# Performance work log

Measured on AMD Instinct MI355X. Metric: run time of the kernel, lower is better.

The kernel has to match this reference:

```python
import jax, jax.numpy as jnp
import numpy as np

N_NODES = 30522
HID = 768
N_EDGES = 488352
B, S = 4, 512
L = 12  # transformer_layers
C = 100  # num classes in pos-neg codebook graph


def setup_inputs() -> dict:
    key = jax.random.key(0)
    ks = jax.random.split(key, 20)
    inp = {}
    inp["word_embs"] = jax.random.normal(ks[0], (N_NODES, HID), dtype=jnp.float32)
    inp["input_ids"] = jax.random.randint(ks[1], (B, S), 0, N_NODES + 1)  # N_NODES = padding row
    inp["class_ids"] = jax.random.randint(ks[2], (B, S), 0, C + 1)
    inp["mask"] = jax.random.randint(ks[3], (B, S, 1), 0, 2).astype(bool)
    inp["co_edge_index"] = jax.random.randint(ks[4], (2, N_EDGES), 0, N_NODES)
    inp["co_edge_weight"] = jax.random.uniform(ks[5], (N_EDGES,), dtype=jnp.float32)
    inp["re_edge_index"] = jax.random.randint(ks[6], (2, N_EDGES), 0, N_NODES)
    inp["re_edge_weight"] = jax.random.uniform(ks[7], (N_EDGES,), dtype=jnp.float32)
    pn_graph = jax.random.uniform(ks[8], (C + 1, N_NODES), dtype=jnp.float32) * 0.01
    inp["pn_graph"] = pn_graph.at[-1].set(0.0)  # padding row of zeros
    sc = 0.02
    inp["co_W"] = jax.random.normal(ks[9], (3, HID, HID), dtype=jnp.float32) * sc
    inp["co_b"] = jnp.zeros((3, HID), jnp.float32)
    inp["re_W"] = jax.random.normal(ks[10], (3, HID, HID), dtype=jnp.float32) * sc
    inp["re_b"] = jnp.zeros((3, HID), jnp.float32)
    inp["pn_W"] = jax.random.normal(ks[11], (HID, HID), dtype=jnp.float32) * sc  # [out,in] 1x1 conv
    inp["pn_b"] = jnp.zeros((HID,), jnp.float32)
    # zero_convs are zero-initialized in the original; use small random so math is non-trivial
    inp["zero_w"] = jax.random.normal(ks[12], (L, HID, HID), dtype=jnp.float32) * sc
    inp["zero_b"] = jnp.zeros((L, HID), jnp.float32)
    inp["zero_w_pos"] = jax.random.normal(ks[13], (L, HID, HID), dtype=jnp.float32) * sc
    inp["zero_b_pos"] = jnp.zeros((L, HID), jnp.float32)
    return inp


def _gcn_layer(x, src, dst, ew, W, b, n):
    # PyG GCNConv: add self-loops (weight 1), symmetric normalization
    deg = jax.ops.segment_sum(ew, dst, num_segments=n) + 1.0
    dinv = jnp.where(deg > 0, jax.lax.rsqrt(deg), 0.0)
    norm = dinv[src] * ew * dinv[dst]  # [E]
    h = x @ W  # [n, H]
    agg = jax.ops.segment_sum(norm[:, None] * h[src], dst, num_segments=n)
    agg = agg + h * (dinv * dinv)[:, None]  # self-loop contribution
    return agg + b


def _gcn_stack(x, edge_index, ew, Ws, bs, ids):
    src, dst = edge_index[0], edge_index[1]
    n = x.shape[0]
    h = x
    acc = None
    for i in range(3):
        h = jax.nn.relu(_gcn_layer(h, src, dst, ew, Ws[i], bs[i], n))
        pad = jnp.concatenate([h, jnp.zeros((1, h.shape[-1]), h.dtype)], axis=0)
        g = pad[ids]  # [B, S, H] gather with padding row
        acc = g if acc is None else acc + g
    return acc / 3.0


def _zero_conv_layers(tok, w, b):
    # 1x1 conv over hidden channels for each of L layers: [B,S,H] x [L,O,H] -> [L,B,S,O]
    return jnp.einsum("bsh,loh->lbso", tok, w) + b[:, None, None, :]


def reference(word_embs, input_ids, class_ids, mask,
              co_edge_index, co_edge_weight, re_edge_index, re_edge_weight,
              pn_graph, co_W, co_b, re_W, re_b, pn_W, pn_b,
              zero_w, zero_b, zero_w_pos, zero_b_pos):
    Bq, Sq = input_ids.shape
    H = word_embs.shape[-1]
    Lq = zero_w.shape[0]
    inv_mask = (~mask).astype(word_embs.dtype)  # [B,S,1]
    zero_pad = jnp.zeros((Lq, Bq, 1, H), word_embs.dtype)

    co = _gcn_stack(word_embs, co_edge_index, co_edge_weight, co_W, co_b, input_ids)  # [B,S,H]
    re = _gcn_stack(word_embs, re_edge_index, re_edge_weight, re_W, re_b, input_ids)

    # NOTE: original uses self.zero_convs (not a separate set) for BOTH co and re
    co_l = _zero_conv_layers(co, zero_w, zero_b) * inv_mask[None]
    re_l = _zero_conv_layers(re, zero_w, zero_b) * inv_mask[None]
    co_l = jnp.concatenate([zero_pad, co_l], axis=2)  # [L,B,S+1,H]
    re_l = jnp.concatenate([zero_pad, re_l], axis=2)

    # PosNegCodebook: 1x1 conv on codebook, then dense-graph matmul, gathered by class
    cb = word_embs @ pn_W.T + pn_b  # [N, H]
    pn = (pn_graph @ cb)[class_ids]  # [B,S,H] (same math as graph[class_ids] @ cb)
    pn_l = _zero_conv_layers(pn, zero_w_pos, zero_b_pos)
    pn_l = jnp.concatenate([zero_pad, pn_l], axis=2)

    return (co_l, re_l, pn_l)
```

## Files before the change

kernel.cpp:

```cpp
#include <hip/hip_runtime.h>
#include <stdint.h>

typedef unsigned int u32;
typedef unsigned short u16;
typedef __attribute__((ext_vector_type(8))) short short8;
typedef __attribute__((ext_vector_type(4))) float f32x4;

#define N_NODESC 30522
#define HIDC 768
#define NEC 488352
#define TOKM 2048
#define LLAY 12
#define NCLS 101
#define M_PAD 30720
#define ZNC (LLAY*HIDC)
#define OUT_SET (LLAY*4*513*HIDC)
#define PN_KCHUNK 512
#define NBLK 120
#define NN1 (N_NODESC+1)
#define G4_LDS 65536
#define G8_LDS 131072

__device__ __forceinline__ float bl(u32 u){ return __uint_as_float(u<<16); }
__device__ __forceinline__ float bh(u32 u){ return __uint_as_float(u & 0xffff0000u); }
__device__ __forceinline__ u32 f2b1(float f){ u32 x=__float_as_uint(f); return (x + 0x7fffu + ((x>>16)&1u))>>16; }
__device__ __forceinline__ u32 pack2(float a, float b){ return f2b1(a) | (f2b1(b)<<16); }

__device__ __forceinline__ void mfma16(f32x4& d, short8 a, short8 b){
  asm volatile("v_mfma_f32_16x16x32_bf16 %0, %1, %2, %0" : "+v"(d) : "v"(a), "v"(b));
}
__device__ __forceinline__ void async16(const void* g, void* l){
  __builtin_amdgcn_global_load_lds((const __attribute__((address_space(1))) u32*)g,
                                   (__attribute__((address_space(3))) u32*)l, 16, 0, 0);
}
__device__ __forceinline__ void em_dec(double d, int& s, float& w){
  unsigned long long b = __double_as_longlong(d);
  s = (int)(u32)b;
  w = __uint_as_float((u32)(b>>32));
}

__global__ void k_invmask(const void* __restrict__ mask, float* __restrict__ invm){
  __shared__ int s_byte, s_flt;
  int t = threadIdx.x;
  const unsigned char* mb = (const unsigned char*)mask;
  const u32* mw = (const u32*)mask;
  int lb=0, lf=0;
  for(int i=t;i<2048;i+=256) if((i&3)!=0 && mb[i]!=0) lb=1;
  for(int i=t;i<512;i+=256) if(mw[i]==0x3F800000u) lf=1;
  if(t==0){ s_byte=0; s_flt=0; }
  __syncthreads();
  if(lb) s_byte=1;
  if(lf) s_flt=1;
  __syncthreads();
  int mode = s_flt ? 2 : (s_byte ? 1 : 0);
  for(int p=t;p<2048;p+=256){
    int mv = (mode==1) ? (int)mb[p] : (int)(mw[p]!=0u);
    invm[p] = mv ? 0.f : 1.f;
  }
}

__global__ void k_needed(const int* __restrict__ ids, u32* __restrict__ needed,
                         u32* __restrict__ need1,
                         int* __restrict__ tmap, int* __restrict__ nxt){
  int p = blockIdx.x*256 + threadIdx.x;
  if(p < TOKM){
    int id = ids[p];
    if(id < N_NODESC){
      needed[id] = 1u;
      need1[id] = 1u;
      need1[N_NODESC + id] = 1u;
      int old = atomicExch(&tmap[id], p);
      nxt[p] = old;
    }
  }
}

__global__ void k_need_expand(const int* __restrict__ coei, const int* __restrict__ reei,
                              const u32* __restrict__ needed, u32* __restrict__ need1){
  int g = blockIdx.y;
  const int* ei = g ? reei : coei;
  int e = blockIdx.x*256 + threadIdx.x;
  if(e < NEC){
    int d = ei[NEC+e];
    if(needed[d]) need1[(size_t)g*N_NODESC + ei[e]] = 1u;
  }
}

__global__ void k_convAll(const float* __restrict__ pnW, const float* __restrict__ zw,
                          const float* __restrict__ zwp,
                          u16* __restrict__ pnwb, u16* __restrict__ zwall){
  const int NP = HIDC*HIDC/2;
  const int NZ = ZNC*HIDC/2;
  int i = blockIdx.x*256 + threadIdx.x;
  if(i < NP){
    ((u32*)pnwb)[i] = pack2(pnW[2*i], pnW[2*i+1]);
  } else if(i < NP + NZ){
    int j = i - NP;
    ((u32*)zwall)[j] = pack2(zw[2*j], zw[2*j+1]);
  } else if(i < NP + 2*NZ){
    int j = i - NP - NZ;
    ((u32*)zwall)[NZ + j] = pack2(zwp[2*j], zwp[2*j+1]);
  }
}
__global__ void k_conv_pad(const float* __restrict__ src, u16* __restrict__ dst, int srcRows, int padRows){
  int i = blockIdx.x*256 + threadIdx.x;
  if(i >= padRows*384) return;
  int row = i/384; int c2 = (i - row*384)*2;
  float lo=0.f, hi=0.f;
  if(row < srcRows){ const float* s = src + (size_t)row*HIDC + c2; lo=s[0]; hi=s[1]; }
  ((u32*)dst)[i] = pack2(lo, hi);
}
__global__ void k_pnb(const float* __restrict__ png, u16* __restrict__ pnb){
  int i = blockIdx.x*256 + threadIdx.x;
  if(i >= 128*(M_PAD/2)) return;
  int row = i/(M_PAD/2); int k2 = (i - row*(M_PAD/2))*2;
  float lo=0.f, hi=0.f;
  if(row < NCLS){
    const float* s = png + (size_t)row*N_NODESC;
    if(k2 < N_NODESC) lo = s[k2];
    if(k2+1 < N_NODESC) hi = s[k2+1];
  }
  ((u32*)pnb)[i] = pack2(lo, hi);
}
__global__ void k_transposeW2(const float* __restrict__ coW, const float* __restrict__ reW,
                              u16* __restrict__ Wt2){
  int g = blockIdx.y;
  int i = blockIdx.x*256 + threadIdx.x;
  if(i >= 3*HIDC*384) return;
  const float* W = g ? reW : coW;
  int mat = i/(HIDC*384); int rem = i - mat*HIDC*384;
  int n = rem/384; int kd = rem - n*384;
  const float* Wm = W + (size_t)mat*HIDC*HIDC;
  float lo = Wm[(size_t)(2*kd)*HIDC + n];
  float hi = Wm[(size_t)(2*kd+1)*HIDC + n];
  ((u32*)Wt2)[(size_t)g*3*HIDC*384 + (size_t)mat*HIDC*384 + (size_t)n*384 + kd] = pack2(lo, hi);
}

__global__ void k_degcnt2(const int* __restrict__ coei, const int* __restrict__ reei,
                          const float* __restrict__ coew, const float* __restrict__ reew,
                          float* __restrict__ deg2, int* __restrict__ cnt2){
  int g = blockIdx.y;
  const int* ei = g ? reei : coei;
  const float* ew = g ? reew : coew;
  int e = blockIdx.x*256 + threadIdx.x;
  if(e < NEC){ int d = ei[NEC+e]; atomicAdd(&deg2[(size_t)g*N_NODESC + d], ew[e]); atomicAdd(&cnt2[(size_t)g*N_NODESC + d], 1); }
}
__global__ void k_scan1(const int* __restrict__ cnt2, int* __restrict__ part2,
                        const float* __restrict__ deg2,
                        float* __restrict__ dinvA, float* __restrict__ dinvB){
  __shared__ int wt[4];
  int g = blockIdx.y, b = blockIdx.x, t = threadIdx.x;
  int lane = t & 63, w = t >> 6;
  int i = b*256 + t;
  if(i < N_NODESC){
    float d = deg2[(size_t)g*N_NODESC + i] + 1.f;
    dinvA[(size_t)g*N_NODESC + i] = rsqrtf(d);
    dinvB[(size_t)g*N_NODESC + i] = 1.f/d;
  }
  int v = (i < N_NODESC) ? cnt2[(size_t)g*N_NODESC + i] : 0;
  int x = v;
  #pragma unroll
  for(int off=1; off<64; off<<=1){ int y = __shfl_up(x, off); if(lane>=off) x += y; }
  if(lane==63) wt[w] = x;
  __syncthreads();
  if(t==0) part2[g*NBLK + b] = wt[0]+wt[1]+wt[2]+wt[3];
}
__global__ void k_scan2(int* __restrict__ part2, int* __restrict__ rp2){
  __shared__ int w0tot;
  int g = blockIdx.x, t = threadIdx.x;
  int lane = t & 63, w = t >> 6;
  int v = (t < NBLK) ? part2[g*NBLK + t] : 0;
  int x = v;
  #pragma unroll
  for(int off=1; off<64; off<<=1){ int y = __shfl_up(x, off); if(lane>=off) x += y; }
  if(w==0 && lane==63) w0tot = x;
  __syncthreads();
  int incl = x + (w ? w0tot : 0);
  int excl = incl - v;
  if(t < NBLK) part2[g*NBLK + t] = excl;
  if(t == 127) rp2[(size_t)g*NN1 + N_NODESC] = incl;
}
__global__ void k_scan3(const int* __restrict__ cnt2, const int* __restrict__ part2,
                        int* __restrict__ rp2, int* __restrict__ cur2){
  __shared__ int wt[4];
  int g = blockIdx.y, b = blockIdx.x, t = threadIdx.x;
  int lane = t & 63, w = t >> 6;
  int i = b*256 + t;
  int v = (i < N_NODESC) ? cnt2[(size_t)g*N_NODESC + i] : 0;
  int x = v;
  #pragma unroll
  for(int off=1; off<64; off<<=1){ int y = __shfl_up(x, off); if(lane>=off) x += y; }
  if(lane==63) wt[w] = x;
  __syncthreads();
  int wpre = 0;
  #pragma unroll
  for(int j=0;j<4;j++) if(j<w) wpre += wt[j];
  int excl = x - v + wpre + part2[g*NBLK + b];
  if(i < N_NODESC){ rp2[(size_t)g*NN1 + i] = excl; cur2[(size_t)g*N_NODESC + i] = excl; }
}
__global__ void k_scatter2(const int* __restrict__ coei, const int* __restrict__ reei,
                           const float* __restrict__ coew, const float* __restrict__ reew,
                           const float* __restrict__ dinvA, int* __restrict__ cur2,
                           float2* __restrict__ emeta){
  int g = blockIdx.y;
  const int* ei = g ? reei : coei;
  const float* ew = g ? reew : coew;
  int e = blockIdx.x*256 + threadIdx.x;
  if(e < NEC){
    int s = ei[e], d = ei[NEC+e];
    int pos = atomicAdd(&cur2[(size_t)g*N_NODESC + d], 1);
    float nrm = dinvA[(size_t)g*N_NODESC + s]*ew[e]*dinvA[(size_t)g*N_NODESC + d];
    emeta[(size_t)g*NEC + pos] = make_float2(__int_as_float(s), nrm);
  }
}

__global__ __launch_bounds__(256)
void k_spmm(const u16* __restrict__ hW, const int* __restrict__ rp,
            const float2* __restrict__ emeta, const float* __restrict__ dinv2,
            const float* __restrict__ bias, u16* __restrict__ hout,
            const u32* __restrict__ needed,
            const int* __restrict__ tmap, const int* __restrict__ nxt,
            float2* __restrict__ tokf, u16* __restrict__ tokb, int phase){
  int v = blockIdx.x*4 + (threadIdx.x>>6);
  if(v >= N_NODESC) return;
  if(needed && !needed[v]) return;
  int lane = threadIdx.x & 63;
  const u32* H = (const u32*)hW;
  const double* em8 = (const double*)emeta;
  float acc[12];
  #pragma unroll
  for(int q=0;q<12;q++) acc[q]=0.f;
  int e0 = rp[v], e1 = rp[v+1];
  int e = e0;
  for(; e+8<=e1; e+=8){
    int s[8]; float w[8];
    #pragma unroll
    for(int j=0;j<8;j++) em_dec(__builtin_nontemporal_load(em8+e+j), s[j], w[j]);
    const u32* r[8];
    #pragma unroll
    for(int j=0;j<8;j++) r[j] = H + (size_t)s[j]*384 + lane;
    u32 u[8][6];
    #pragma unroll
    for(int j=0;j<8;j++){
      #pragma unroll
      for(int q=0;q<6;q++) u[j][q] = r[j][q*64];
    }
    #pragma unroll
    for(int q=0;q<6;q++){
      acc[2*q]   += w[0]*bl(u[0][q]) + w[1]*bl(u[1][q]) + w[2]*bl(u[2][q]) + w[3]*bl(u[3][q]);
      acc[2*q+1] += w[0]*bh(u[0][q]) + w[1]*bh(u[1][q]) + w[2]*bh(u[2][q]) + w[3]*bh(u[3][q]);
      acc[2*q]   += w[4]*bl(u[4][q]) + w[5]*bl(u[5][q]) + w[6]*bl(u[6][q]) + w[7]*bl(u[7][q]);
      acc[2*q+1] += w[4]*bh(u[4][q]) + w[5]*bh(u[5][q]) + w[6]*bh(u[6][q]) + w[7]*bh(u[7][q]);
    }
  }
  for(; e+4<=e1; e+=4){
    int s0,s1,s2,s3; float w0,w1,w2,w3;
    em_dec(__builtin_nontemporal_load(em8+e  ), s0, w0);
    em_dec(__builtin_nontemporal_load(em8+e+1), s1, w1);
    em_dec(__builtin_nontemporal_load(em8+e+2), s2, w2);
    em_dec(__builtin_nontemporal_load(em8+e+3), s3, w3);
    const u32* r0 = H + (size_t)s0*384 + lane;
    const u32* r1 = H + (size_t)s1*384 + lane;
    const u32* r2 = H + (size_t)s2*384 + lane;
    const u32* r3 = H + (size_t)s3*384 + lane;
    u32 u0[6],u1[6],u2[6],u3[6];
    #pragma unroll
    for(int q=0;q<6;q++){ u0[q]=r0[q*64]; u1[q]=r1[q*64]; u2[q]=r2[q*64]; u3[q]=r3[q*64]; }
    #pragma unroll
    for(int q=0;q<6;q++){
      acc[2*q]   += w0*bl(u0[q]) + w1*bl(u1[q]) + w2*bl(u2[q]) + w3*bl(u3[q]);
      acc[2*q+1] += w0*bh(u0[q]) + w1*bh(u1[q]) + w2*bh(u2[q]) + w3*bh(u3[q]);
    }
  }
  for(; e<e1; ++e){
    int ss; float ww;
    em_dec(__builtin_nontemporal_load(em8+e), ss, ww);
    const u32* r = H + (size_t)ss*384 + lane;
    #pragma unroll
    for(int q=0;q<6;q++){ u32 u = r[q*64]; acc[2*q] += ww*bl(u); acc[2*q+1] += ww*bh(u); }
  }
  { float wgt = dinv2[v];
    const u32* r = H + (size_t)v*384 + lane;
    #pragma unroll
    for(int q=0;q<6;q++){ u32 u = r[q*64]; acc[2*q] += wgt*bl(u); acc[2*q+1] += wgt*bh(u); }
  }
  const float2* B2 = (const float2*)bias;
  u32 wv[6];
  #pragma unroll
  for(int q=0;q<6;q++){
    float2 bb = B2[lane + 64*q];
    float x0 = fmaxf(acc[2*q]+bb.x, 0.f);
    float x1 = fmaxf(acc[2*q+1]+bb.y, 0.f);
    wv[q] = pack2(x0, x1);
  }
  if(phase != 2){
    u32* O = (u32*)hout + (size_t)v*384 + lane;
    #pragma unroll
    for(int q=0;q<6;q++) O[q*64] = wv[q];
  }
  int p = tmap[v];
  while(p >= 0){
    float2* TF = tokf + (size_t)p*384 + lane;
    if(phase == 0){
      #pragma unroll
      for(int q=0;q<6;q++)
        TF[q*64] = make_float2(bl(wv[q])*(1.f/3.f), bh(wv[q])*(1.f/3.f));
    } else if(phase == 1){
      #pragma unroll
      for(int q=0;q<6;q++){
        float2 c = TF[q*64];
        c.x += bl(wv[q])*(1.f/3.f); c.y += bh(wv[q])*(1.f/3.f);
        TF[q*64] = c;
      }
    } else {
      u32* TB = (u32*)tokb + (size_t)p*384 + lane;
      #pragma unroll
      for(int q=0;q<6;q++){
        float2 c = TF[q*64];
        c.x += bl(wv[q])*(1.f/3.f); c.y += bh(wv[q])*(1.f/3.f);
        TB[q*64] = pack2(c.x, c.y);
      }
    }
    p = nxt[p];
  }
}

__global__ void k_gather_pn(const float* __restrict__ GT, const int* __restrict__ cids, u16* __restrict__ tokb){
  int d = blockIdx.x*256 + threadIdx.x;
  if(d >= TOKM*384) return;
  int p = d/384, q = d - p*384;
  int cid = cids[p];
  float lo = GT[(size_t)(2*q)*128 + cid];
  float hi = GT[(size_t)(2*q+1)*128 + cid];
  ((u32*)tokb)[d] = pack2(lo, hi);
}

__global__ void k_zerocol(float* __restrict__ out){
  int i = blockIdx.x*256 + threadIdx.x;
  if(i >= 3*LLAY*4*HIDC) return;
  int set = i/(LLAY*4*HIDC); int rem = i - set*(LLAY*4*HIDC);
  int l = rem/(4*HIDC); int rem2 = rem - l*(4*HIDC);
  int b = rem2/HIDC; int o = rem2 - b*HIDC;
  out[(size_t)set*OUT_SET + (size_t)(l*4+b)*513*HIDC + o] = 0.f;
}

__device__ __forceinline__ void g_split(int ntM, int ntN, int& bm, int& bn){
  int nwg = ntM*ntN;
  int bid = (int)blockIdx.x;
  int wg = (bid & 7)*(nwg>>3) + (bid>>3);
  if(ntN <= ntM){ bm = wg/ntN; bn = wg - bm*ntN; }
  else          { bn = wg/ntM; bm = wg - bn*ntM; }
}

#define G8_AOFF(b) ((b)*65536)
#define G8_BOFF(b) ((b)*65536 + 32768)

__device__ __forceinline__ void g8_stage(const u16* __restrict__ src, int ldk, int g0, int kt,
                                         char* half_base, int tid){
  const int lane = tid & 63;
  const int csw = ((lane&7) ^ (lane>>3)) << 3;
  const u16* s0 = src + (size_t)(g0 + (tid>>3))*ldk + (kt + csw);
  const u16* s1 = src + (size_t)(g0 + 64 + (tid>>3))*ldk + (kt + csw);
  async16(s0, half_base + (size_t)tid*16);
  async16(s1, half_base + 8192 + (size_t)tid*16);
}

__device__ __forceinline__ void g8_core(const u16* __restrict__ A, const u16* __restrict__ Bt,
                                        int K, int m0, int n0,
                                        f32x4 (&acc)[8][4], char* LDS, int tid){
  const int lane = tid & 63;
  const int wid = tid >> 6;
  const int wr = wid >> 2, wc = wid & 3;
  const int NK = K >> 6;

  g8_stage(Bt, K, n0,      0, LDS + G8_BOFF(0),         tid);
  g8_stage(Bt, K, n0+128,  0, LDS + G8_BOFF(0) + 16384, tid);
  g8_stage(A,  K, m0,      0, LDS + G8_AOFF(0),         tid);
  g8_stage(A,  K, m0+128,  0, LDS + G8_AOFF(0) + 16384, tid);
  g8_stage(Bt, K, n0,     64, LDS + G8_BOFF(1),         tid);
  g8_stage(Bt, K, n0+128, 64, LDS + G8_BOFF(1) + 16384, tid);
  asm volatile("s_waitcnt vmcnt(4)" ::: "memory");
  __builtin_amdgcn_sched_barrier(0);
  __builtin_amdgcn_s_barrier();
  __builtin_amdgcn_sched_barrier(0);

  short8 bf8[8];
  for(int T=0; T<NK; ++T){
    const int buf = T & 1;
    const char* Ab = LDS + G8_AOFF(buf) + wr*16384;
    const char* Bb = LDS + G8_BOFF(buf) + (wc>>1)*16384;
    #pragma unroll
    for(int q=0; q<4; ++q){
      if(q==0){
        #pragma unroll
        for(int n=0;n<4;n++){
          #pragma unroll
          for(int kk=0;kk<2;kk++){
            int row = ((wc&1)<<6) + (n<<4) + (lane&15);
            int cb = ((kk<<6) + ((lane>>4)<<4)) ^ ((lane&7)<<4);
            bf8[n*2+kk] = *(const short8*)(Bb + row*128 + cb);
          }
        }
      }
      short8 af[2][2];
      #pragma unroll
      for(int j=0;j<2;j++){
        #pragma unroll
        for(int kk=0;kk<2;kk++){
          int row = ((2*q+j)<<4) + (lane&15);
          int cb = ((kk<<6) + ((lane>>4)<<4)) ^ ((lane&7)<<4);
          af[j][kk] = *(const short8*)(Ab + row*128 + cb);
        }
      }
      if(q==0 && T+1<NK) g8_stage(A,  K, m0,      (T+1)<<6, LDS + G8_AOFF((T+1)&1),         tid);
      if(q==1 && T+1<NK) g8_stage(A,  K, m0+128,  (T+1)<<6, LDS + G8_AOFF((T+1)&1) + 16384, tid);
      if(q==2 && T+2<NK) g8_stage(Bt, K, n0,      (T+2)<<6, LDS + G8_BOFF(buf),             tid);
      if(q==3 && T+2<NK) g8_stage(Bt, K, n0+128,  (T+2)<<6, LDS + G8_BOFF(buf) + 16384,     tid);
      if(q==3){
        if(T <= NK-3)      asm volatile("s_waitcnt vmcnt(4)" ::: "memory");
        else if(T == NK-2) asm volatile("s_waitcnt vmcnt(0)" ::: "memory");
      }
      __builtin_amdgcn_sched_barrier(0);
      __builtin_amdgcn_s_barrier();
      __builtin_amdgcn_sched_barrier(0);
      __builtin_amdgcn_s_setprio(1);
      #pragma unroll
      for(int j=0;j<2;j++){
        #pragma unroll
        for(int n=0;n<4;n++){
          #pragma unroll
          for(int kk=0;kk<2;kk++) mfma16(acc[2*q+j][n], af[j][kk], bf8[n*2+kk]);
        }
      }
      __builtin_amdgcn_s_setprio(0);
      __builtin_amdgcn_sched_barrier(0);
      __builtin_amdgcn_s_barrier();
      __builtin_amdgcn_sched_barrier(0);
    }
  }
}

__global__ __launch_bounds__(512,2)
void gemm8p_zc(const u16* __restrict__ TOKALL, const u16* __restrict__ ZWALL,
               const float* __restrict__ zb, const float* __restrict__ zbp,
               const float* __restrict__ invm, float* __restrict__ out){
  extern __shared__ char LDS[];
  const int set = blockIdx.z;
  const u16* A  = TOKALL + (size_t)set*TOKM*HIDC;
  const u16* Bt = ZWALL + (set==2 ? (size_t)ZNC*HIDC : 0);
  const float* bias = (set==2) ? zbp : zb;
  const bool use_mask = (set != 2);
  float* o = out + (size_t)set*OUT_SET;

  const int tid = threadIdx.x;
  const int lane = tid & 63;
  const int wid = tid >> 6;
  const int wr = wid >> 2, wc = wid & 3;
  int bm, bn;
  g_split(TOKM>>8, ZNC>>8, bm, bn);
  const int m0 = bm << 8, n0 = bn << 8;

  f32x4 acc[8][4];
  f32x4 zv = {0.f,0.f,0.f,0.f};
  #pragma unroll
  for(int m=0;m<8;m++){
    #pragma unroll
    for(int n=0;n<4;n++) acc[m][n] = zv;
  }
  g8_core(A, Bt, HIDC, m0, n0, acc, LDS, tid);

  const int l = n0 / HIDC;
  const int oc0 = n0 - l*HIDC;
  const int lo = lane & 15, hi = lane >> 4;

  #pragma unroll
  for(int pass=0; pass<2; ++pass){
    __syncthreads();
    if(wr == pass){
      #pragma unroll
      for(int m=0;m<8;m++){
        #pragma unroll
        for(int n=0;n<4;n++){
          int col = (wc<<6) + (n<<4) + lo;
          float badd = bias[n0 + col];
          #pragma unroll
          for(int r=0;r<4;r++){
            int lr = (m<<4) + (hi<<2) + r;
            *(float*)(LDS + (size_t)lr*1024 + ((col<<2) ^ ((lr&7)<<4))) = acc[m][n][r] + badd;
          }
        }
      }
    }
    __syncthreads();
    #pragma unroll
    for(int i=0;i<16;i++){
      int lr = (i<<3) + wid;
      int rr = m0 + (pass<<7) + lr;
      int b = rr >> 9, s = rr & 511;
      f32x4 v = *(const f32x4*)(LDS + (size_t)lr*1024 + ((lane<<4) ^ ((lr&7)<<4)));
      if(use_mask){ float w = invm[rr]; v = v * w; }
      *(f32x4*)(o + (size_t)((l*4+b)*513 + (s+1))*HIDC + oc0 + (lane<<2)) = v;
    }
  }
}

#define G4_ABUF(b) ((b)*32768)
#define G4_BBUF(b) ((b)*32768 + 16384)

__device__ __forceinline__ void g4_stage(const u16* __restrict__ src, int ldk, int g0, int kt,
                                         char* base, int tid){
  const int lane = tid & 63;
  const int csw = ((lane&7) ^ (lane>>3)) << 3;
  const int r = tid >> 3;
  #pragma unroll
  for(int h=0; h<4; ++h)
    async16(src + (size_t)(g0 + h*32 + r)*ldk + (kt + csw), base + h*4096 + (size_t)tid*16);
}

__device__ __forceinline__ void g4_core(const u16* __restrict__ A, const u16* __restrict__ Bt,
                                        int K, int m0, int n0,
                                        f32x4 (&acc)[4][4], char* LDS, int tid){
  const int lane = tid & 63;
  const int wid = tid >> 6;
  const int wr = wid >> 1, wc = wid & 1;
  const int NK = K >> 6;

  g4_stage(A,  K, m0,  0, LDS + G4_ABUF(0), tid);
  g4_stage(Bt, K, n0,  0, LDS + G4_BBUF(0), tid);
  g4_stage(A,  K, m0, 64, LDS + G4_ABUF(1), tid);
  g4_stage(Bt, K, n0, 64, LDS + G4_BBUF(1), tid);

  short8 af[4][2], bf[4][2];
  for(int T=0; T<NK; ++T){
    const int buf = T & 1;
    const char* Ab = LDS + G4_ABUF(buf) + wr*8192;
    const char* Bb = LDS + G4_BBUF(buf) + wc*8192;
    if(T+1 < NK) asm volatile("s_waitcnt vmcnt(8)" ::: "memory");
    else         asm volatile("s_waitcnt vmcnt(0)" ::: "memory");
    __builtin_amdgcn_sched_barrier(0);
    __builtin_amdgcn_s_barrier();
    __builtin_amdgcn_sched_barrier(0);
    #pragma unroll
    for(int m=0;m<4;m++){
      #pragma unroll
      for(int kk=0;kk<2;kk++){
        int row = (m<<4) + (lane&15);
        int cb = ((kk<<6) + ((lane>>4)<<4)) ^ ((lane&7)<<4);
        af[m][kk] = *(const short8*)(Ab + row*128 + cb);
        bf[m][kk] = *(const short8*)(Bb + row*128 + cb);
      }
    }
    asm volatile("s_waitcnt lgkmcnt(0)" ::: "memory");
    __builtin_amdgcn_sched_barrier(0);
    __builtin_amdgcn_s_setprio(1);
    #pragma unroll
    for(int m=0;m<2;m++){
      #pragma unroll
      for(int n=0;n<4;n++){
        #pragma unroll
        for(int kk=0;kk<2;kk++) mfma16(acc[m][n], af[m][kk], bf[n][kk]);
      }
    }
    __builtin_amdgcn_s_setprio(0);
    __builtin_amdgcn_sched_barrier(0);
    __builtin_amdgcn_s_barrier();
    __builtin_amdgcn_sched_barrier(0);
    if(T+2 < NK){
      g4_stage(A,  K, m0, (T+2)<<6, LDS + G4_ABUF(buf), tid);
      g4_stage(Bt, K, n0, (T+2)<<6, LDS + G4_BBUF(buf), tid);
    }
    __builtin_amdgcn_s_setprio(1);
    #pragma unroll
    for(int m=2;m<4;m++){
      #pragma unroll
      for(int n=0;n<4;n++){
        #pragma unroll
        for(int kk=0;kk<2;kk++) mfma16(acc[m][n], af[m][kk], bf[n][kk]);
      }
    }
    __builtin_amdgcn_s_setprio(0);
    __builtin_amdgcn_sched_barrier(0);
  }
}

template<int MODE>
__global__ __launch_bounds__(256,2)
void gemm4p_bf16(const u16* __restrict__ A, const u16* __restrict__ Bt,
                 int M, int N, int K,
                 u16* __restrict__ outB, const float* __restrict__ bias){
  extern __shared__ char LDS[];
  const int tid = threadIdx.x;
  const int lane = tid & 63;
  const int wid = tid >> 6;
  const int wr = wid >> 1, wc = wid & 1;
  int bm, bn;
  g_split(M>>7, N>>7, bm, bn);
  const int m0 = bm << 7, n0 = bn << 7;

  f32x4 acc[4][4];
  f32x4 zv = {0.f,0.f,0.f,0.f};
  #pragma unroll
  for(int m=0;m<4;m++){
    #pragma unroll
    for(int n=0;n<4;n++) acc[m][n] = zv;
  }
  g4_core(A, Bt, K, m0, n0, acc, LDS, tid);

  const int rbase = (lane>>4)<<2;
  const int cbase = lane & 15;
  #pragma unroll
  for(int m=0;m<4;m++){
    int row0 = m0 + (wr<<6) + (m<<4) + rbase;
    #pragma unroll
    for(int n=0;n<4;n++){
      int col = n0 + (wc<<6) + (n<<4) + cbase;
      #pragma unroll
      for(int r=0;r<4;r++){
        float v = acc[m][n][r];
        if(MODE==2) v += bias[row0+r];
        outB[(size_t)(row0+r)*N + col] = (u16)f2b1(v);
      }
    }
  }
}

__global__ __launch_bounds__(256,2)
void gemm_splitk(const u16* __restrict__ A, const u16* __restrict__ Bt,
                 int M, int N, int K, float* __restrict__ outF, int kchunk){
  __shared__ u16 As[128*64];
  __shared__ u16 Bs[128*64];
  const int t = threadIdx.x;
  const int lane = t & 63;
  const int w = t >> 6;
  const int wr = w >> 1, wc = w & 1;
  int nchunks = (K + kchunk - 1)/kchunk;
  int bm = (int)blockIdx.x / nchunks;
  int ch = (int)blockIdx.x - bm*nchunks;
  int k0 = ch*kchunk, k1 = k0 + kchunk; if(k1 > K) k1 = K;
  const int m0 = bm << 7, n0 = 0;

  f32x4 zv = {0.f,0.f,0.f,0.f};
  f32x4 acc[4][4];
  #pragma unroll
  for(int m=0;m<4;m++){
    #pragma unroll
    for(int n=0;n<4;n++) acc[m][n] = zv;
  }
  const int srow = t >> 3;
  const int scol = (t & 7) << 3;
  const u16* Ag = A + (size_t)(m0 + srow)*K + scol;
  const u16* Bg = Bt + (size_t)(n0 + srow)*K + scol;
  u16* Al = &As[t*8];
  u16* Bl = &Bs[t*8];

  for(int kt=k0; kt<k1; kt+=64){
    __syncthreads();
    #pragma unroll
    for(int i=0;i<4;i++){
      async16(Ag + (size_t)(i*32)*K + kt, Al + i*2048);
      async16(Bg + (size_t)(i*32)*K + kt, Bl + i*2048);
    }
    __syncthreads();
    #pragma unroll
    for(int kk=0; kk<64; kk+=32){
      const int ko = kk + ((lane>>4)<<3);
      short8 af[4], bfv[4];
      #pragma unroll
      for(int m=0;m<4;m++) af[m] = *(const short8*)&As[((wr<<6)+(m<<4)+(lane&15))*64 + ko];
      #pragma unroll
      for(int n=0;n<4;n++) bfv[n] = *(const short8*)&Bs[((wc<<6)+(n<<4)+(lane&15))*64 + ko];
      #pragma unroll
      for(int m=0;m<4;m++){
        #pragma unroll
        for(int n=0;n<4;n++) mfma16(acc[m][n], af[m], bfv[n]);
      }
    }
  }
  const int rbase = (lane>>4)<<2;
  const int cbase = lane & 15;
  #pragma unroll
  for(int m=0;m<4;m++){
    int row0 = m0 + (wr<<6) + (m<<4) + rbase;
    #pragma unroll
    for(int n=0;n<4;n++){
      int col = n0 + (wc<<6) + (n<<4) + cbase;
      #pragma unroll
      for(int r=0;r<4;r++) atomicAdd(&outF[(size_t)(row0+r)*N + col], acc[m][n][r]);
    }
  }
}

extern "C" void kernel_launch(void* const* d_in, const int* in_sizes, int n_in,
                              void* d_out, int out_size, void* d_ws, size_t ws_size,
                              hipStream_t stream){
  const float* word  = (const float*)d_in[0];
  const int*   ids   = (const int*)d_in[1];
  const int*   cids  = (const int*)d_in[2];
  const void*  mask  = d_in[3];
  const int*   co_ei = (const int*)d_in[4];
  const float* co_ew = (const float*)d_in[5];
  const int*   re_ei = (const int*)d_in[6];
  const float* re_ew = (const float*)d_in[7];
  const float* png   = (const float*)d_in[8];
  const float* co_W  = (const float*)d_in[9];
  const float* co_b  = (const float*)d_in[10];
  const float* re_W  = (const float*)d_in[11];
  const float* re_b  = (const float*)d_in[12];
  const float* pn_W  = (const float*)d_in[13];
  const float* pn_b  = (const float*)d_in[14];
  const float* zw    = (const float*)d_in[15];
  const float* zb    = (const float*)d_in[16];
  const float* zwp   = (const float*)d_in[17];
  const float* zbp   = (const float*)d_in[18];
  float* out = (float*)d_out;

  hipFuncSetAttribute((const void*)gemm4p_bf16<0>, hipFuncAttributeMaxDynamicSharedMemorySize, G4_LDS);
  hipFuncSetAttribute((const void*)gemm4p_bf16<2>, hipFuncAttributeMaxDynamicSharedMemorySize, G4_LDS);
  hipFuncSetAttribute((const void*)gemm8p_zc,      hipFuncAttributeMaxDynamicSharedMemorySize, G8_LDS);

  char* wsb = (char*)d_ws;
  size_t off = 0;
  auto alloc = [&](size_t bytes)->void*{ void* p = wsb + off; off += (bytes + 255) & ~(size_t)255; return p; };
  u16* WORDB = (u16*)alloc((size_t)M_PAD*HIDC*2);
  u16* BUFB  = (u16*)alloc((size_t)M_PAD*HIDC*2);
  u16* BUFX  = (u16*)alloc((size_t)M_PAD*HIDC*2);
  u16* ZWALL = (u16*)alloc((size_t)2*ZNC*HIDC*2);
  u16* WT2   = (u16*)alloc((size_t)2*3*HIDC*HIDC*2);
  u16* PNWB  = (u16*)alloc((size_t)HIDC*HIDC*2);
  u16* PNB   = (u16*)alloc((size_t)128*M_PAD*2);
  u16* TOKALL= (u16*)alloc((size_t)3*TOKM*HIDC*2);
  float2* TOKF = (float2*)alloc((size_t)TOKM*HIDC*4);
  float* GT   = (float*)alloc((size_t)HIDC*128*4);
  float* DEG2 = (float*)alloc((size_t)2*N_NODESC*4);
  int*   CNT2 = (int*)alloc((size_t)2*N_NODESC*4);
  float* DINVA = (float*)alloc((size_t)2*N_NODESC*4);
  float* DINVB = (float*)alloc((size_t)2*N_NODESC*4);
  int*   RP2  = (int*)alloc((size_t)2*NN1*4);
  int*   CUR2 = (int*)alloc((size_t)2*N_NODESC*4);
  int*   PART2= (int*)alloc((size_t)2*NBLK*4);
  float2* EMETA=(float2*)alloc((size_t)2*NEC*8);
  u32*   NEED = (u32*)alloc((size_t)N_NODESC*4);
  u32*   NEED1= (u32*)alloc((size_t)2*N_NODESC*4);
  int*   TMAP = (int*)alloc((size_t)N_NODESC*4);
  int*   NXT  = (int*)alloc((size_t)TOKM*4);
  float* INVM = (float*)alloc((size_t)TOKM*4);
  (void)ws_size; (void)in_sizes; (void)n_in; (void)out_size;

  const int GD_TOK = (TOKM*384 + 255)/256;
  const int GD_E   = (NEC + 255)/256;
  const int SPMM_GD  = (N_NODESC + 3)/4;
  const int PN_NCHUNKS = M_PAD/PN_KCHUNK;
  const int G_PN  = (HIDC/128)*PN_NCHUNKS;
  const int G4_GCN = (M_PAD/128)*(HIDC/128);
  const int G4_CBT = (HIDC/128)*(M_PAD/128);
  const int G8_ZC  = (TOKM/256)*(ZNC/256);
  const int NCONV  = HIDC*HIDC/2 + 2*(ZNC*HIDC/2);

  hipMemsetAsync(NEED, 0, (size_t)N_NODESC*4, stream);
  hipMemsetAsync(NEED1, 0, (size_t)2*N_NODESC*4, stream);
  hipMemsetAsync(TMAP, 0xFF, (size_t)N_NODESC*4, stream);
  hipMemsetAsync(DEG2, 0, (size_t)2*N_NODESC*4, stream);
  hipMemsetAsync(CNT2, 0, (size_t)2*N_NODESC*4, stream);
  hipMemsetAsync(TOKALL, 0, (size_t)2*TOKM*HIDC*2, stream);
  k_invmask<<<1,256,0,stream>>>(mask, INVM);
  k_needed<<<(TOKM+255)/256,256,0,stream>>>(ids, NEED, NEED1, TMAP, NXT);
  k_need_expand<<<dim3(GD_E,2),256,0,stream>>>(co_ei, re_ei, NEED, NEED1);
  k_convAll<<<(NCONV + 255)/256,256,0,stream>>>(pn_W, zw, zwp, PNWB, ZWALL);
  k_conv_pad<<<(M_PAD*384 + 255)/256,256,0,stream>>>(word, WORDB, N_NODESC, M_PAD);
  k_transposeW2<<<dim3((3*HIDC*384 + 255)/256, 2),256,0,stream>>>(co_W, re_W, WT2);

  k_degcnt2<<<dim3(GD_E,2),256,0,stream>>>(co_ei, re_ei, co_ew, re_ew, DEG2, CNT2);
  k_scan1<<<dim3(NBLK,2),256,0,stream>>>(CNT2, PART2, DEG2, DINVA, DINVB);
  k_scan2<<<2,128,0,stream>>>(PART2, RP2);
  k_scan3<<<dim3(NBLK,2),256,0,stream>>>(CNT2, PART2, RP2, CUR2);
  k_scatter2<<<dim3(GD_E,2),256,0,stream>>>(co_ei, re_ei, co_ew, re_ew, DINVA, CUR2, EMETA);

  gemm4p_bf16<2><<<G4_CBT,256,G4_LDS,stream>>>(PNWB, WORDB, HIDC, M_PAD, HIDC, BUFX, pn_b);
  k_pnb<<<(128*(M_PAD/2) + 255)/256,256,0,stream>>>(png, PNB);
  hipMemsetAsync(GT, 0, (size_t)HIDC*128*4, stream);
  gemm_splitk<<<G_PN,256,0,stream>>>(BUFX, PNB, HIDC, 128, M_PAD, GT, PN_KCHUNK);
  k_gather_pn<<<GD_TOK,256,0,stream>>>(GT, cids, TOKALL + (size_t)2*TOKM*HIDC);

  auto run_graph = [&](int g, const float* bf, u16* tokb){
    const int* rp = RP2 + (size_t)g*NN1;
    const float2* em = EMETA + (size_t)g*NEC;
    const float* di2 = DINVB + (size_t)g*N_NODESC;
    const u16* X = WORDB;
    for(int i=0;i<3;i++){
      gemm4p_bf16<0><<<G4_GCN,256,G4_LDS,stream>>>(X, WT2 + ((size_t)g*3 + i)*HIDC*HIDC,
                                                   M_PAD, HIDC, HIDC, BUFB, nullptr);
      const u32* flt = (i==2) ? NEED : (i==1 ? NEED1 + (size_t)g*N_NODESC : nullptr);
      k_spmm<<<SPMM_GD,256,0,stream>>>(BUFB, rp, em, di2, bf + i*HIDC, BUFX, flt,
                                       TMAP, NXT, TOKF, tokb, i);
      X = BUFX;
    }
  };
  run_graph(0, co_b, TOKALL);
  run_graph(1, re_b, TOKALL + (size_t)TOKM*HIDC);

  dim3 zgrid(G8_ZC, 1, 3);
  gemm8p_zc<<<zgrid,512,G8_LDS,stream>>>(TOKALL, ZWALL, zb, zbp, INVM, out);
  k_zerocol<<<(3*LLAY*4*HIDC + 255)/256,256,0,stream>>>(out);
}
```

Baseline: 1.123 ms.

## Batch co/re GCN graphs into shared launches and fold small prep kernels

The co and re GCN stacks now run together: each layer's GEMM and SpMM are single launches over both graphs (grid z/y selects the graph) when the workspace is big enough, using doubled intermediate buffers. The k_pnb conversion is merged into k_convAll and k_zerocol is folded into the zero-conv GEMM epilogue. Several memsets are combined into one contiguous memset. The intent is fewer launches and better GPU fill for the small filtered SpMM phases. The cost is a larger workspace, with a fallback to the per-graph path when it is too small.

```diff
diff --git a/kernel.cpp b/kernel.cpp
--- a/kernel.cpp
+++ b/kernel.cpp
@@ -87,10 +87,12 @@
 }
 
 __global__ void k_convAll(const float* __restrict__ pnW, const float* __restrict__ zw,
-                          const float* __restrict__ zwp,
-                          u16* __restrict__ pnwb, u16* __restrict__ zwall){
+                          const float* __restrict__ zwp, const float* __restrict__ png,
+                          u16* __restrict__ pnwb, u16* __restrict__ zwall,
+                          u16* __restrict__ pnb){
   const int NP = HIDC*HIDC/2;
   const int NZ = ZNC*HIDC/2;
+  const int NB = 128*(M_PAD/2);
   int i = blockIdx.x*256 + threadIdx.x;
   if(i < NP){
     ((u32*)pnwb)[i] = pack2(pnW[2*i], pnW[2*i+1]);
@@ -100,6 +102,16 @@
   } else if(i < NP + 2*NZ){
     int j = i - NP - NZ;
     ((u32*)zwall)[NZ + j] = pack2(zwp[2*j], zwp[2*j+1]);
+  } else if(i < NP + 2*NZ + NB){
+    int j = i - NP - 2*NZ;
+    int row = j/(M_PAD/2); int k2 = (j - row*(M_PAD/2))*2;
+    float lo=0.f, hi=0.f;
+    if(row < NCLS){
+      const float* s = png + (size_t)row*N_NODESC;
+      if(k2 < N_NODESC) lo = s[k2];
+      if(k2+1 < N_NODESC) hi = s[k2+1];
+    }
+    ((u32*)pnb)[j] = pack2(lo, hi);
   }
 }
 __global__ void k_conv_pad(const float* __restrict__ src, u16* __restrict__ dst, int srcRows, int padRows){
@@ -109,18 +121,6 @@
   float lo=0.f, hi=0.f;
   if(row < srcRows){ const float* s = src + (size_t)row*HIDC + c2; lo=s[0]; hi=s[1]; }
   ((u32*)dst)[i] = pack2(lo, hi);
-}
-__global__ void k_pnb(const float* __restrict__ png, u16* __restrict__ pnb){
-  int i = blockIdx.x*256 + threadIdx.x;
-  if(i >= 128*(M_PAD/2)) return;
-  int row = i/(M_PAD/2); int k2 = (i - row*(M_PAD/2))*2;
-  float lo=0.f, hi=0.f;
-  if(row < NCLS){
-    const float* s = png + (size_t)row*N_NODESC;
-    if(k2 < N_NODESC) lo = s[k2];
-    if(k2+1 < N_NODESC) hi = s[k2+1];
-  }
-  ((u32*)pnb)[i] = pack2(lo, hi);
 }
 __global__ void k_transposeW2(const float* __restrict__ coW, const float* __restrict__ reW,
                               u16* __restrict__ Wt2){
@@ -215,18 +215,31 @@
 }
 
 __global__ __launch_bounds__(256)
-void k_spmm(const u16* __restrict__ hW, const int* __restrict__ rp,
-            const float2* __restrict__ emeta, const float* __restrict__ dinv2,
-            const float* __restrict__ bias, u16* __restrict__ hout,
-            const u32* __restrict__ needed,
-            const int* __restrict__ tmap, const int* __restrict__ nxt,
-            float2* __restrict__ tokf, u16* __restrict__ tokb, int phase){
+void k_spmm2(const u16* __restrict__ hWb, size_t hstride,
+             const int* __restrict__ rp2, const float2* __restrict__ emb,
+             const float* __restrict__ dinvb,
+             const float* __restrict__ bias_co, const float* __restrict__ bias_re,
+             u16* __restrict__ houtb, size_t ostride,
+             const u32* __restrict__ needarr, const u32* __restrict__ need1,
+             const int* __restrict__ tmap, const int* __restrict__ nxt,
+             float2* __restrict__ tokfb, size_t tfstride,
+             u16* __restrict__ tokall, int phase, int gbase){
+  const int g = gbase + blockIdx.y;
+  const u16* hW = hWb + (size_t)blockIdx.y*hstride;
+  const int* rp = rp2 + (size_t)g*NN1;
+  const double* em8 = (const double*)(emb + (size_t)g*NEC);
+  const float* dinv2 = dinvb + (size_t)g*N_NODESC;
+  const float* bias = (g ? bias_re : bias_co) + phase*HIDC;
+  u16* hout = houtb + (size_t)blockIdx.y*ostride;
+  const u32* flt = (phase==2) ? needarr : (phase==1 ? need1 + (size_t)g*N_NODESC : nullptr);
+  float2* tokf = tokfb + (size_t)blockIdx.y*tfstride;
+  u16* tokb = tokall + (size_t)g*TOKM*HIDC;
+
   int v = blockIdx.x*4 + (threadIdx.x>>6);
   if(v >= N_NODESC) return;
-  if(needed && !needed[v]) return;
+  if(flt && !flt[v]) return;
   int lane = threadIdx.x & 63;
   const u32* H = (const u32*)hW;
-  const double* em8 = (const double*)emeta;
   float acc[12];
   #pragma unroll
   for(int q=0;q<12;q++) acc[q]=0.f;
@@ -335,15 +348,6 @@
   ((u32*)tokb)[d] = pack2(lo, hi);
 }
 
-__global__ void k_zerocol(float* __restrict__ out){
-  int i = blockIdx.x*256 + threadIdx.x;
-  if(i >= 3*LLAY*4*HIDC) return;
-  int set = i/(LLAY*4*HIDC); int rem = i - set*(LLAY*4*HIDC);
-  int l = rem/(4*HIDC); int rem2 = rem - l*(4*HIDC);
-  int b = rem2/HIDC; int o = rem2 - b*HIDC;
-  out[(size_t)set*OUT_SET + (size_t)(l*4+b)*513*HIDC + o] = 0.f;
-}
-
 __device__ __forceinline__ void g_split(int ntM, int ntN, int& bm, int& bn){
   int nwg = ntM*ntN;
   int bid = (int)blockIdx.x;
@@ -500,6 +504,10 @@
       f32x4 v = *(const f32x4*)(LDS + (size_t)lr*1024 + ((lane<<4) ^ ((lr&7)<<4)));
       if(use_mask){ float w = invm[rr]; v = v * w; }
       *(f32x4*)(o + (size_t)((l*4+b)*513 + (s+1))*HIDC + oc0 + (lane<<2)) = v;
+      if(s == 0){
+        f32x4 z4 = {0.f,0.f,0.f,0.f};
+        *(f32x4*)(o + (size_t)((l*4+b)*513)*HIDC + oc0 + (lane<<2)) = z4;
+      }
     }
   }
 }
@@ -583,9 +591,8 @@
   }
 }
 
-template<int MODE>
 __global__ __launch_bounds__(256,2)
-void gemm4p_bf16(const u16* __restrict__ A, const u16* __restrict__ Bt,
+void gemm4p_bias(const u16* __restrict__ A, const u16* __restrict__ Bt,
                  int M, int N, int K,
                  u16* __restrict__ outB, const float* __restrict__ bias){
   extern __shared__ char LDS[];
@@ -616,10 +623,51 @@
       int col = n0 + (wc<<6) + (n<<4) + cbase;
       #pragma unroll
       for(int r=0;r<4;r++){
-        float v = acc[m][n][r];
-        if(MODE==2) v += bias[row0+r];
+        float v = acc[m][n][r] + bias[row0+r];
         outB[(size_t)(row0+r)*N + col] = (u16)f2b1(v);
       }
+    }
+  }
+}
+
+__global__ __launch_bounds__(256,2)
+void gemm4p_gcn(const u16* __restrict__ Xb, size_t xstride,
+                const u16* __restrict__ wt2, int layer,
+                u16* __restrict__ outb, size_t ostride, int gbase){
+  extern __shared__ char LDS[];
+  const int g = gbase + blockIdx.z;
+  const u16* A = Xb + (size_t)blockIdx.z*xstride;
+  const u16* Bt = wt2 + ((size_t)g*3 + layer)*HIDC*HIDC;
+  u16* outB = outb + (size_t)blockIdx.z*ostride;
+
+  const int tid = threadIdx.x;
+  const int lane = tid & 63;
+  const int wid = tid >> 6;
+  const int wr = wid >> 1, wc = wid & 1;
+  int bm, bn;
+  g_split(M_PAD>>7, HIDC>>7, bm, bn);
+  const int m0 = bm << 7, n0 = bn << 7;
+
+  f32x4 acc[4][4];
+  f32x4 zv = {0.f,0.f,0.f,0.f};
+  #pragma unroll
+  for(int m=0;m<4;m++){
+    #pragma unroll
+    for(int n=0;n<4;n++) acc[m][n] = zv;
+  }
+  g4_core(A, Bt, HIDC, m0, n0, acc, LDS, tid);
+
+  const int rbase = (lane>>4)<<2;
+  const int cbase = lane & 15;
+  #pragma unroll
+  for(int m=0;m<4;m++){
+    int row0 = m0 + (wr<<6) + (m<<4) + rbase;
+    #pragma unroll
+    for(int n=0;n<4;n++){
+      int col = n0 + (wc<<6) + (n<<4) + cbase;
+      #pragma unroll
+      for(int r=0;r<4;r++)
+        outB[(size_t)(row0+r)*HIDC + col] = (u16)f2b1(acc[m][n][r]);
     }
   }
 }
@@ -714,33 +762,39 @@
   const float* zbp   = (const float*)d_in[18];
   float* out = (float*)d_out;
 
-  hipFuncSetAttribute((const void*)gemm4p_bf16<0>, hipFuncAttributeMaxDynamicSharedMemorySize, G4_LDS);
-  hipFuncSetAttribute((const void*)gemm4p_bf16<2>, hipFuncAttributeMaxDynamicSharedMemorySize, G4_LDS);
-  hipFuncSetAttribute((const void*)gemm8p_zc,      hipFuncAttributeMaxDynamicSharedMemorySize, G8_LDS);
+  hipFuncSetAttribute((const void*)gemm4p_bias, hipFuncAttributeMaxDynamicSharedMemorySize, G4_LDS);
+  hipFuncSetAttribute((const void*)gemm4p_gcn,  hipFuncAttributeMaxDynamicSharedMemorySize, G4_LDS);
+  hipFuncSetAttribute((const void*)gemm8p_zc,   hipFuncAttributeMaxDynamicSharedMemorySize, G8_LDS);
+
+  const size_t MH = (size_t)M_PAD*HIDC;
+  const size_t TFS = (size_t)TOKM*384;
+  const bool batched = ws_size >= ((size_t)340 << 20);
 
   char* wsb = (char*)d_ws;
   size_t off = 0;
   auto alloc = [&](size_t bytes)->void*{ void* p = wsb + off; off += (bytes + 255) & ~(size_t)255; return p; };
-  u16* WORDB = (u16*)alloc((size_t)M_PAD*HIDC*2);
-  u16* BUFB  = (u16*)alloc((size_t)M_PAD*HIDC*2);
-  u16* BUFX  = (u16*)alloc((size_t)M_PAD*HIDC*2);
+  u16* WORDB = (u16*)alloc(MH*2);
+  u16* BUFB  = (u16*)alloc(MH*2*(batched?2:1));
+  u16* BUFX  = (u16*)alloc(MH*2*(batched?2:1));
   u16* ZWALL = (u16*)alloc((size_t)2*ZNC*HIDC*2);
   u16* WT2   = (u16*)alloc((size_t)2*3*HIDC*HIDC*2);
   u16* PNWB  = (u16*)alloc((size_t)HIDC*HIDC*2);
   u16* PNB   = (u16*)alloc((size_t)128*M_PAD*2);
   u16* TOKALL= (u16*)alloc((size_t)3*TOKM*HIDC*2);
-  float2* TOKF = (float2*)alloc((size_t)TOKM*HIDC*4);
-  float* GT   = (float*)alloc((size_t)HIDC*128*4);
+  float2* TOKF = (float2*)alloc(TFS*8*(batched?2:1));
+  size_t zg0 = off;
+  u32*   NEED = (u32*)alloc((size_t)N_NODESC*4);
+  u32*   NEED1= (u32*)alloc((size_t)2*N_NODESC*4);
   float* DEG2 = (float*)alloc((size_t)2*N_NODESC*4);
   int*   CNT2 = (int*)alloc((size_t)2*N_NODESC*4);
+  float* GT   = (float*)alloc((size_t)HIDC*128*4);
+  size_t zg_bytes = off - zg0;
   float* DINVA = (float*)alloc((size_t)2*N_NODESC*4);
   float* DINVB = (float*)alloc((size_t)2*N_NODESC*4);
   int*   RP2  = (int*)alloc((size_t)2*NN1*4);
   int*   CUR2 = (int*)alloc((size_t)2*N_NODESC*4);
   int*   PART2= (int*)alloc((size_t)2*NBLK*4);
   float2* EMETA=(float2*)alloc((size_t)2*NEC*8);
-  u32*   NEED = (u32*)alloc((size_t)N_NODESC*4);
-  u32*   NEED1= (u32*)alloc((size_t)2*N_NODESC*4);
   int*   TMAP = (int*)alloc((size_t)N_NODESC*4);
   int*   NXT  = (int*)alloc((size_t)TOKM*4);
   float* INVM = (float*)alloc((size_t)TOKM*4);
@@ -754,18 +808,15 @@
   const int G4_GCN = (M_PAD/128)*(HIDC/128);
   const int G4_CBT = (HIDC/128)*(M_PAD/128);
   const int G8_ZC  = (TOKM/256)*(ZNC/256);
-  const int NCONV  = HIDC*HIDC/2 + 2*(ZNC*HIDC/2);
-
-  hipMemsetAsync(NEED, 0, (size_t)N_NODESC*4, stream);
-  hipMemsetAsync(NEED1, 0, (size_t)2*N_NODESC*4, stream);
+  const int NCONVALL = HIDC*HIDC/2 + 2*(ZNC*HIDC/2) + 128*(M_PAD/2);
+
+  hipMemsetAsync(wsb + zg0, 0, zg_bytes, stream);
   hipMemsetAsync(TMAP, 0xFF, (size_t)N_NODESC*4, stream);
-  hipMemsetAsync(DEG2, 0, (size_t)2*N_NODESC*4, stream);
-  hipMemsetAsync(CNT2, 0, (size_t)2*N_NODESC*4, stream);
   hipMemsetAsync(TOKALL, 0, (size_t)2*TOKM*HIDC*2, stream);
   k_invmask<<<1,256,0,stream>>>(mask, INVM);
   k_needed<<<(TOKM+255)/256,256,0,stream>>>(ids, NEED, NEED1, TMAP, NXT);
   k_need_expand<<<dim3(GD_E,2),256,0,stream>>>(co_ei, re_ei, NEED, NEED1);
-  k_convAll<<<(NCONV + 255)/256,256,0,stream>>>(pn_W, zw, zwp, PNWB, ZWALL);
+  k_convAll<<<(NCONVALL + 255)/256,256,0,stream>>>(pn_W, zw, zwp, png, PNWB, ZWALL, PNB);
   k_conv_pad<<<(M_PAD*384 + 255)/256,256,0,stream>>>(word, WORDB, N_NODESC, M_PAD);
   k_transposeW2<<<dim3((3*HIDC*384 + 255)/256, 2),256,0,stream>>>(co_W, re_W, WT2);
 
@@ -775,30 +826,31 @@
   k_scan3<<<dim3(NBLK,2),256,0,stream>>>(CNT2, PART2, RP2, CUR2);
   k_scatter2<<<dim3(GD_E,2),256,0,stream>>>(co_ei, re_ei, co_ew, re_ew, DINVA, CUR2, EMETA);
 
-  gemm4p_bf16<2><<<G4_CBT,256,G4_LDS,stream>>>(PNWB, WORDB, HIDC, M_PAD, HIDC, BUFX, pn_b);
-  k_pnb<<<(128*(M_PAD/2) + 255)/256,256,0,stream>>>(png, PNB);
-  hipMemsetAsync(GT, 0, (size_t)HIDC*128*4, stream);
+  gemm4p_bias<<<G4_CBT,256,G4_LDS,stream>>>(PNWB, WORDB, HIDC, M_PAD, HIDC, BUFX, pn_b);
   gemm_splitk<<<G_PN,256,0,stream>>>(BUFX, PNB, HIDC, 128, M_PAD, GT, PN_KCHUNK);
   k_gather_pn<<<GD_TOK,256,0,stream>>>(GT, cids, TOKALL + (size_t)2*TOKM*HIDC);
 
-  auto run_graph = [&](int g, const float* bf, u16* tokb){
-    const int* rp = RP2 + (size_t)g*NN1;
-    const float2* em = EMETA + (size_t)g*NEC;
-    const float* di2 = DINVB + (size_t)g*N_NODESC;
-    const u16* X = WORDB;
+  if(batched){
     for(int i=0;i<3;i++){
-      gemm4p_bf16<0><<<G4_GCN,256,G4_LDS,stream>>>(X, WT2 + ((size_t)g*3 + i)*HIDC*HIDC,
-                                                   M_PAD, HIDC, HIDC, BUFB, nullptr);
-      const u32* flt = (i==2) ? NEED : (i==1 ? NEED1 + (size_t)g*N_NODESC : nullptr);
-      k_spmm<<<SPMM_GD,256,0,stream>>>(BUFB, rp, em, di2, bf + i*HIDC, BUFX, flt,
-                                       TMAP, NXT, TOKF, tokb, i);
-      X = BUFX;
-    }
-  };
-  run_graph(0, co_b, TOKALL);
-  run_graph(1, re_b, TOKALL + (size_t)TOKM*HIDC);
+      gemm4p_gcn<<<dim3(G4_GCN,1,2),256,G4_LDS,stream>>>(
+          (i==0)? WORDB : BUFX, (i==0)? 0 : MH, WT2, i, BUFB, MH, 0);
+      k_spmm2<<<dim3(SPMM_GD,2),256,0,stream>>>(
+          BUFB, MH, RP2, EMETA, DINVB, co_b, re_b, BUFX, MH,
+          NEED, NEED1, TMAP, NXT, TOKF, TFS, TOKALL, i, 0);
+    }
+  } else {
+    for(int g=0; g<2; ++g){
+      const u16* X = WORDB;
+      for(int i=0;i<3;i++){
+        gemm4p_gcn<<<dim3(G4_GCN,1,1),256,G4_LDS,stream>>>(X, 0, WT2, i, BUFB, 0, g);
+        k_spmm2<<<dim3(SPMM_GD,1),256,0,stream>>>(
+            BUFB, 0, RP2, EMETA, DINVB, co_b, re_b, BUFX, 0,
+            NEED, NEED1, TMAP, NXT, TOKF, 0, TOKALL, i, g);
+        X = BUFX;
+      }
+    }
+  }
 
   dim3 zgrid(G8_ZC, 1, 3);
   gemm8p_zc<<<zgrid,512,G8_LDS,stream>>>(TOKALL, ZWALL, zb, zbp, INVM, out);
-  k_zerocol<<<(3*LLAY*4*HIDC + 255)/256,256,0,stream>>>(out);
-}
+}
```

Measured after the change: 1.088 ms (median of 2 runs). 1.03x faster.
